# Kernel optimization log

Hardware: AMD Instinct MI355X
Metric: run time of the kernel (lower is better)

## Reference

```python
import jax, jax.numpy as jnp
import numpy as np

PI = float(np.pi)
BN_EPS = 1e-3
LN_EPS = 1e-5


def ssslu(x, shape, bias):
    # x * (sin(softsign(x) * shape*pi/2) + (bias + 1))
    s = x / (1.0 + jnp.abs(x))
    return x * (jnp.sin(s * (shape * PI / 2.0)) + (bias + 1.0))


def bn(x, g, b, m, v):
    inv = (g / jnp.sqrt(v + BN_EPS))[None, :, None, None]
    return (x - m[None, :, None, None]) * inv + b[None, :, None, None]


def conv2d(x, w, bias=None, pad=0):
    y = jax.lax.conv_general_dilated(x, w, (1, 1), [(pad, pad), (pad, pad)],
                                     dimension_numbers=('NCHW', 'OIHW', 'NCHW'))
    if bias is not None:
        y = y + bias[None, :, None, None]
    return y


def ln_silu(v):
    # LayerNorm (unit weight, zero bias) over last axis, then SiLU
    mu = jnp.mean(v, axis=-1, keepdims=True)
    var = jnp.mean(jnp.square(v - mu), axis=-1, keepdims=True)
    h = (v - mu) / jnp.sqrt(var + LN_EPS)
    return h * jax.nn.sigmoid(h)


def _forward(x, w_qkv, g_qkv, b_qkv, m_qkv, v_qkv,
             w_co, g_co, b_co, m_co, v_co,
             w_b1, bias_b1, g_b1, b_b1, m_b1, v_b1,
             w_b2, bias_b2, g_b2, b_b2, m_b2, v_b2):
    B, C, H, W = x.shape
    Q = (w_qkv.shape[0] - C) // 2
    # qkv Conv block: conv1x1 -> SSSLU(-3, 0.3) -> BN
    t = bn(ssslu(conv2d(x, w_qkv, pad=0), -3.0, 0.3), g_qkv, b_qkv, m_qkv, v_qkv)
    xq, xk, xv = jnp.split(t, [Q, 2 * Q], axis=1)
    # max-pooled Q/K rows and columns -> [B*Q, W] / [B*Q, H]
    qw = jnp.max(xq, axis=2).reshape(B * Q, W)
    kw = jnp.max(xk, axis=2).reshape(B * Q, W)
    qh = jnp.max(xq, axis=3).reshape(B * Q, H)
    kh = jnp.max(xk, axis=3).reshape(B * Q, H)
    # xaw[i,b] = max_a qw[i,a]*kw[i,b]; xah[i,a] = max_b qh[i,a]*kh[i,b]
    xaw = jnp.max(qw[:, :, None] * kw[:, None, :], axis=1)  # [BQ, W]
    xah = jnp.max(qh[:, :, None] * kh[:, None, :], axis=2)  # [BQ, H]
    xaw = ln_silu(xaw)
    xah = ln_silu(xah)
    xa = (xah[:, :, None] * xaw[:, None, :]).reshape(B, Q, H, W)
    # co: SSSLUConv(Q+C -> Q): conv3x3 -> BN -> SSSLU(1.0, 0)
    xa = jnp.concatenate([xa, xv], axis=1)
    xa = ssslu(bn(conv2d(xa, w_co, pad=1), g_co, b_co, m_co, v_co), 1.0, 0.0)
    # back[0]: Conv(Q -> C, k3, bias): conv -> SSSLU(-3, 0.3) -> BN
    xa = bn(ssslu(conv2d(xa, w_b1, bias_b1, pad=1), -3.0, 0.3), g_b1, b_b1, m_b1, v_b1)
    # back[1]: SSSLUConv(C -> C, k1, bias): conv -> BN -> SSSLU(0.8, 0)
    xa = ssslu(bn(conv2d(xa, w_b2, bias_b2, pad=0), g_b2, b_b2, m_b2, v_b2), 0.8, 0.0)
    # back[2]: Sigmoid; source returns the gate itself
    return jax.nn.sigmoid(xa)


def setup_inputs() -> dict:
    B, C, Q, H, W = 16, 256, 256, 64, 64
    key = jax.random.key(0)
    ks = jax.random.split(key, 32)

    def w_init(k, o, i, kh, kw):
        return jax.random.normal(k, (o, i, kh, kw), jnp.float32) * (1.0 / np.sqrt(i * kh * kw))

    def bn_params(k, c):
        k1, k2, k3, k4 = jax.random.split(k, 4)
        g = jax.random.uniform(k1, (c,), jnp.float32, 0.5, 1.5)
        b = jax.random.normal(k2, (c,), jnp.float32) * 0.1
        m = jax.random.normal(k3, (c,), jnp.float32) * 0.1
        v = jax.random.uniform(k4, (c,), jnp.float32, 0.5, 1.5)
        return g, b, m, v

    x = jax.random.normal(ks[0], (B, C, H, W), jnp.float32)
    w_qkv = w_init(ks[1], 2 * Q + C, C, 1, 1)
    g_qkv, b_qkv, m_qkv, v_qkv = bn_params(ks[2], 2 * Q + C)
    w_co = w_init(ks[3], Q, Q + C, 3, 3)
    g_co, b_co, m_co, v_co = bn_params(ks[4], Q)
    w_b1 = w_init(ks[5], C, Q, 3, 3)
    bias_b1 = jax.random.normal(ks[6], (C,), jnp.float32) * 0.05
    g_b1, b_b1, m_b1, v_b1 = bn_params(ks[7], C)
    w_b2 = w_init(ks[8], C, C, 1, 1)
    bias_b2 = jax.random.normal(ks[9], (C,), jnp.float32) * 0.05
    g_b2, b_b2, m_b2, v_b2 = bn_params(ks[10], C)
    return dict(x=x, w_qkv=w_qkv, g_qkv=g_qkv, b_qkv=b_qkv, m_qkv=m_qkv, v_qkv=v_qkv,
                w_co=w_co, g_co=g_co, b_co=b_co, m_co=m_co, v_co=v_co,
                w_b1=w_b1, bias_b1=bias_b1, g_b1=g_b1, b_b1=b_b1, m_b1=m_b1, v_b1=v_b1,
                w_b2=w_b2, bias_b2=bias_b2, g_b2=g_b2, b_b2=b_b2, m_b2=m_b2, v_b2=v_b2)


def reference(x, w_qkv, g_qkv, b_qkv, m_qkv, v_qkv,
              w_co, g_co, b_co, m_co, v_co,
              w_b1, bias_b1, g_b1, b_b1, m_b1, v_b1,
              w_b2, bias_b2, g_b2, b_b2, m_b2, v_b2):
    return _forward(x, w_qkv, g_qkv, b_qkv, m_qkv, v_qkv,
                    w_co, g_co, b_co, m_co, v_co,
                    w_b1, bias_b1, g_b1, b_b1, m_b1, v_b1,
                    w_b2, bias_b2, g_b2, b_b2, m_b2, v_b2)
```

## Files before the change

kernel.cpp:

```cpp
#include <hip/hip_runtime.h>
#include <hip/hip_bf16.h>
#include <math.h>

#define PI_F 3.14159265358979323846f

typedef unsigned short u16;
typedef unsigned int   u32;
typedef float    f32x4 __attribute__((ext_vector_type(4)));
typedef _Float16 f16x8 __attribute__((ext_vector_type(8)));
typedef u16      u16x8 __attribute__((ext_vector_type(8)));
typedef u16      u16x4 __attribute__((ext_vector_type(4)));

__device__ __forceinline__ u16 f2h(float f){ union{ _Float16 h; u16 u; } c; c.h = (_Float16)f; return c.u; }
__device__ __forceinline__ float h2f(u16 u){ union{ u16 u; _Float16 h; } c; c.u = u; return (float)c.h; }

__device__ __forceinline__ void gl16(const void* g, void* l){
  __builtin_amdgcn_global_load_lds((const __attribute__((address_space(1))) u32*)g,
                                   (__attribute__((address_space(3))) u32*)l, 16, 0, 0);
}

__device__ __forceinline__ int SWZ(int r){ return (r>>1)&3; }

__device__ __forceinline__ float wred_max(float v){
#pragma unroll
  for (int m = 32; m; m >>= 1) v = fmaxf(v, __shfl_xor(v, m));
  return v;
}
__device__ __forceinline__ float wred_min(float v){
#pragma unroll
  for (int m = 32; m; m >>= 1) v = fminf(v, __shfl_xor(v, m));
  return v;
}
__device__ __forceinline__ float wred_sum(float v){
#pragma unroll
  for (int m = 32; m; m >>= 1) v += __shfl_xor(v, m);
  return v;
}

__device__ __forceinline__ float ssslu_f(float x, float shp, float bp1){
  float s = x / (1.0f + fabsf(x));
  return x * (__sinf(s * shp) + bp1);
}

__device__ __forceinline__ float epi_val(float v, float4 p, float shp, float bp1, int ORDER, bool SIG){
  v += p.w;
  if (ORDER == 0){ v = ssslu_f(v, shp, bp1); v = (v - p.z) * p.x + p.y; }
  else           { v = (v - p.z) * p.x + p.y; v = ssslu_f(v, shp, bp1); }
  if (SIG) v = 1.f / (1.f + __expf(-v));
  return v;
}

__device__ __forceinline__ f16x8 mul8h(u16x8 a, u16x8 b){
  union{ u16x8 u; f16x8 h; } A, B; A.u = a; B.u = b;
  return A.h * B.h;
}

__global__ __launch_bounds__(256)
void xpose_k(const float* __restrict__ X, u16* __restrict__ XH)
{
  __shared__ u16 L[16384];
  const int tid = threadIdx.x;
  const int b = blockIdx.x >> 6, h = blockIdx.x & 63;
  const float* xp = X + (size_t)b * 256 * 4096 + h * 64;
#pragma unroll
  for (int i = 0; i < 16; ++i){
    int ci = i * 16 + (tid >> 4);
    int w4 = (tid & 15) * 4;
    float4 v = *(const float4*)(xp + (size_t)ci * 4096 + w4);
    int sw = 4 * ((ci >> 3) & 15);
    u16x4 d;
    d[0] = f2h(v.x); d[1] = f2h(v.y); d[2] = f2h(v.z); d[3] = f2h(v.w);
    *(u16x4*)&L[ci * 64 + (w4 ^ sw)] = d;
  }
  __syncthreads();
  u16* out = XH + (((size_t)b * 4096 + (size_t)h * 64) << 8);
#pragma unroll
  for (int it = 0; it < 8; ++it){
    int w   = it * 8 + (tid >> 5);
    int m   = tid & 31;
    int ci0 = m * 8;
    int base = (w & ~3) ^ (4 * (m & 15));
    int wl   = w & 3;
    u16x8 o;
#pragma unroll
    for (int k = 0; k < 8; ++k)
      o[k] = L[(ci0 + k) * 64 + base + wl];
    *(u16x8*)&out[w * 256 + ci0] = o;
  }
}

template<int CI_T, bool CAT>
__global__ __launch_bounds__(256, 2)
void conv3_mfma(const u16* __restrict__ Apk, const u16* __restrict__ Bg,
                u16* __restrict__ DstH, const float4* __restrict__ pp,
                const u16* __restrict__ xahT_, const u16* __restrict__ xawT_,
                float shp, float bp1, int ORDER)
{
  constexpr int NCC = CI_T / 32;
  constexpr int NIT = NCC * 3;
  __shared__ __align__(16) u16 sAB[37248];

  const int tid  = threadIdx.x;
  const int lane = tid & 63;
  const int wv   = tid >> 6;
  const int wn   = wv;
  const int l15  = lane & 15, l4 = lane >> 4;

  const int bx  = blockIdx.x;
  const int bid = (bx & 7) * 32 + (bx >> 3);
  const int b   = bid >> 4;
  const int r0  = (bid & 15) * 4;
  const int m0  = blockIdx.y * 128;

  if (tid < 192){
    int rr = tid >> 5, rem = tid & 31;
    int wp = (rem & 16) ? 65 : 0;
    *(u32*)&sAB[24576 + rr * 2112 + wp * 32 + (rem & 15) * 2] = 0;
  }
  if (r0 == 0)
    for (int i = tid; i < 1056; i += 256) *(u32*)&sAB[24576 + i * 2] = 0;
  if (r0 == 60)
    for (int i = tid; i < 1056; i += 256) *(u32*)&sAB[24576 + 5 * 2112 + i * 2] = 0;

  const int rA = tid >> 2, s4 = tid & 3;
  const u32 offA0 = ((u32)rA * CI_T + ((s4 ^ SWZ(rA)) << 3)) * 2;
  const u32 offA1 = ((u32)(rA + 64) * CI_T + ((s4 ^ SWZ(rA + 64)) << 3)) * 2;
  const u32 offB  = (((u32)rA << 8) + ((s4 ^ SWZ(rA + 1)) << 3)) * 2;

  auto STAGE_A = [&](int it2){
    int d2 = it2 % 3, c2 = it2 / 3;
    u16* dst = &sAB[(it2 & 1) * 12288 + wv * 512];
    const char* pa = (const char*)(Apk + ((size_t)(d2 * 3 * 256) + m0) * CI_T + c2 * 32);
#pragma unroll
    for (int j2 = 0; j2 < 3; ++j2){
      gl16(pa + offA0, dst + j2 * 4096);
      gl16(pa + offA1, dst + j2 * 4096 + 2048);
      pa += (size_t)256 * CI_T * 2;
    }
  };
  auto STAGE_B = [&](int c2){
#pragma unroll
    for (int j = 0; j < 6; ++j){
      int hh = r0 - 1 + j;
      if ((unsigned)hh >= 64u) continue;
      if (CAT && c2 < 8){
        int w = rA, s = s4;
        int ci0 = c2 * 32 + ((s ^ SWZ(w + 1)) << 3);
        u16x8 vh = *(const u16x8*)&xahT_[((b * 64 + hh) << 8) + ci0];
        u16x8 vw = *(const u16x8*)&xawT_[((b * 64 + w ) << 8) + ci0];
        *(f16x8*)&sAB[24576 + j * 2112 + (w + 1) * 32 + s * 8] = mul8h(vh, vw);
      } else {
        int cio = CAT ? (c2 * 32 - 256) : (c2 * 32);
        const char* pb = (const char*)(Bg + (((size_t)b * 4096 + (size_t)hh * 64) << 8) + cio);
        gl16(pb + offB, &sAB[24576 + j * 2112 + 32 + wv * 512]);
      }
    }
  };

  f32x4 acc[8][4];
#pragma unroll
  for (int i = 0; i < 8; ++i)
#pragma unroll
    for (int j = 0; j < 4; ++j){ acc[i][j][0]=0.f; acc[i][j][1]=0.f; acc[i][j][2]=0.f; acc[i][j][3]=0.f; }

  const char* lds = (const char*)sAB;
  const u32 aoff = (u32)l15 * 64 + (u32)((l4 ^ ((l15 >> 1) & 3)) << 4);
  const char* ab0 = lds + aoff;
  const char* ab1 = lds + aoff + 24576;
  const u32 bcom = 49152u + (u32)wn * 4224;
  const char* bb0 = lds + bcom + (u32)(l15 + 0) * 64 + (u32)((l4 ^ (((l15 + 0) >> 1) & 3)) << 4);
  const char* bb1 = lds + bcom + (u32)(l15 + 1) * 64 + (u32)((l4 ^ (((l15 + 1) >> 1) & 3)) << 4);
  const char* bb2 = lds + bcom + (u32)(l15 + 2) * 64 + (u32)((l4 ^ (((l15 + 2) >> 1) & 3)) << 4);

  STAGE_A(0);

  for (int c = 0; c < NCC; ++c){
#pragma unroll
    for (int d = 0; d < 3; ++d){
      const int it = 3 * c + d;
      if (it + 1 < NIT) STAGE_A(it + 1);
      if (d == 0){ STAGE_B(c); __syncthreads(); }

      const char* ab = ((c + d) & 1) ? ab1 : ab0;
#pragma unroll
      for (int dw = 0; dw < 3; ++dw){
        const char* bp = (dw == 0) ? bb0 : (dw == 1) ? bb1 : bb2;
        f16x8 afr[8], bfr[4];
#pragma unroll
        for (int fm = 0; fm < 8; ++fm)
          afr[fm] = *(const f16x8*)(ab + dw * 8192 + fm * 1024);
#pragma unroll
        for (int fn = 0; fn < 4; ++fn)
          bfr[fn] = *(const f16x8*)(bp + d * 4224 + fn * 1024);
        __builtin_amdgcn_s_setprio(1);
#pragma unroll
        for (int fm = 0; fm < 8; ++fm)
#pragma unroll
          for (int fn = 0; fn < 4; ++fn)
            acc[fm][fn] = __builtin_amdgcn_mfma_f32_16x16x32_f16(afr[fm], bfr[fn], acc[fm][fn], 0, 0, 0);
        __builtin_amdgcn_s_setprio(0);
      }
      __syncthreads();
    }
  }

  const int h = r0 + wn;
#pragma unroll
  for (int fm = 0; fm < 8; ++fm){
    const int cobase = m0 + fm * 16 + 4 * l4;
    float4 P0 = pp[cobase], P1 = pp[cobase+1], P2 = pp[cobase+2], P3 = pp[cobase+3];
#pragma unroll
    for (int fn = 0; fn < 4; ++fn){
      int w = fn * 16 + l15;
      float v0 = epi_val(acc[fm][fn][0], P0, shp, bp1, ORDER, false);
      float v1 = epi_val(acc[fm][fn][1], P1, shp, bp1, ORDER, false);
      float v2 = epi_val(acc[fm][fn][2], P2, shp, bp1, ORDER, false);
      float v3 = epi_val(acc[fm][fn][3], P3, shp, bp1, ORDER, false);
      uint2 st;
      st.x = (u32)f2h(v0) | ((u32)f2h(v1) << 16);
      st.y = (u32)f2h(v2) | ((u32)f2h(v3) << 16);
      *(uint2*)&DstH[(((size_t)b * 4096 + (size_t)h * 64 + w) << 8) + cobase] = st;
    }
  }
}

template<int EPI>
__global__ __launch_bounds__(512, 2)
void conv1_res(const u16* __restrict__ Apk0, const u16* __restrict__ Bg,
               u16* __restrict__ DstH, float* __restrict__ DstF,
               const float4* __restrict__ pp0,
               float* __restrict__ qhp, float* __restrict__ khp,
               float* __restrict__ qwp, float* __restrict__ kwp,
               float shp, float bp1, int ORDER)
{
  __shared__ __align__(16) u16 AL[65536];
  float* pool = (float*)AL;

  const int tid  = threadIdx.x;
  const int lane = tid & 63;
  const int wv   = tid >> 6;
  const int wm   = wv >> 2;
  const int wn   = wv & 3;
  const int l15  = lane & 15, l4 = lane >> 4;

  const int bx   = blockIdx.x;
  const int bid  = (bx & 7) * 32 + (bx >> 3);
  const int b    = bid >> 4;
  const int hblk = bid & 15;
  const int h0   = hblk * 4;
  const int m0   = (EPI == 0) ? (blockIdx.y * 256) : 0;

  const u16*    Apk = Apk0 + (size_t)m0 * 256;
  const float4* pp  = pp0 + m0;

  {
    const int g0 = tid;
    const int g1 = 512 + tid;
    const int mA0 = g0 >> 2, sA0 = g0 & 3;
    const int mA1 = g1 >> 2, sA1 = g1 & 3;
    const u32 offA0 = ((u32)mA0 * 256 + ((sA0 ^ SWZ(mA0)) << 3)) * 2;
    const u32 offA1 = ((u32)mA1 * 256 + ((sA1 ^ SWZ(mA1)) << 3)) * 2;
#pragma unroll
    for (int c = 0; c < 8; ++c){
      const char* pa = (const char*)(Apk + c * 32);
      gl16(pa + offA0, &AL[c * 8192 + (wv * 64) * 8]);
      gl16(pa + offA1, &AL[c * 8192 + (512 + wv * 64) * 8]);
    }
  }

  const u16* Bp = Bg + (((size_t)b * 4096 + (size_t)(h0 + wn) * 64) << 8) + (l15 << 8) + (l4 << 3);
#define LDB(c, fn) (*(const f16x8*)(Bp + ((fn) * 16 << 8) + (c) * 32))

  f32x4 acc[8][4];
#pragma unroll
  for (int i = 0; i < 8; ++i)
#pragma unroll
    for (int j = 0; j < 4; ++j){ acc[i][j][0]=0.f; acc[i][j][1]=0.f; acc[i][j][2]=0.f; acc[i][j][3]=0.f; }

  f16x8 bn0 = LDB(0, 0), bn1 = LDB(0, 1), bn2 = LDB(0, 2), bn3 = LDB(0, 3);

  __syncthreads();

  const char* abase = (const char*)AL + wm * 8192 + l15 * 64 + ((l4 ^ SWZ(l15)) << 4);

#pragma unroll
  for (int c = 0; c < 8; ++c){
    f16x8 b0 = bn0, b1 = bn1, b2 = bn2, b3 = bn3;
    if (c < 7){
      bn0 = LDB(c + 1, 0); bn1 = LDB(c + 1, 1); bn2 = LDB(c + 1, 2); bn3 = LDB(c + 1, 3);
    }
    f16x8 afr[8];
#pragma unroll
    for (int fm = 0; fm < 8; ++fm)
      afr[fm] = *(const f16x8*)(abase + c * 16384 + fm * 1024);
    __builtin_amdgcn_s_setprio(1);
#pragma unroll
    for (int fm = 0; fm < 8; ++fm){
      acc[fm][0] = __builtin_amdgcn_mfma_f32_16x16x32_f16(afr[fm], b0, acc[fm][0], 0, 0, 0);
      acc[fm][1] = __builtin_amdgcn_mfma_f32_16x16x32_f16(afr[fm], b1, acc[fm][1], 0, 0, 0);
      acc[fm][2] = __builtin_amdgcn_mfma_f32_16x16x32_f16(afr[fm], b2, acc[fm][2], 0, 0, 0);
      acc[fm][3] = __builtin_amdgcn_mfma_f32_16x16x32_f16(afr[fm], b3, acc[fm][3], 0, 0, 0);
    }
    __builtin_amdgcn_s_setprio(0);
  }
#undef LDB

  const int h = h0 + wn;

  if (EPI == 0){
    float* rowp = (blockIdx.y == 0) ? qhp : khp;
    float* colp = (blockIdx.y == 0) ? qwp : kwp;
    __syncthreads();
#pragma unroll
    for (int k = 0; k < 4; ++k){
      if (wn == k){
#pragma unroll
        for (int fm = 0; fm < 8; ++fm){
          const int cl = wm * 128 + fm * 16 + 4 * l4;
          float4 P0 = pp[cl], P1 = pp[cl+1], P2 = pp[cl+2], P3 = pp[cl+3];
          float ev[4][4];
#pragma unroll
          for (int fn = 0; fn < 4; ++fn){
            ev[fn][0] = epi_val(acc[fm][fn][0], P0, shp, bp1, 0, false);
            ev[fn][1] = epi_val(acc[fm][fn][1], P1, shp, bp1, 0, false);
            ev[fn][2] = epi_val(acc[fm][fn][2], P2, shp, bp1, 0, false);
            ev[fn][3] = epi_val(acc[fm][fn][3], P3, shp, bp1, 0, false);
          }
#pragma unroll
          for (int r = 0; r < 4; ++r){
            float mv = fmaxf(fmaxf(ev[0][r], ev[1][r]), fmaxf(ev[2][r], ev[3][r]));
            mv = fmaxf(mv, __shfl_xor(mv, 1));
            mv = fmaxf(mv, __shfl_xor(mv, 2));
            mv = fmaxf(mv, __shfl_xor(mv, 4));
            mv = fmaxf(mv, __shfl_xor(mv, 8));
            if (l15 == 0)
              rowp[(((b << 8) | (cl + r)) << 6) + h] = mv;
          }
#pragma unroll
          for (int fn = 0; fn < 4; ++fn)
#pragma unroll
            for (int r = 0; r < 4; ++r){
              int idx = ((cl + r) << 6) + fn * 16 + l15;
              pool[idx] = (k == 0) ? ev[fn][r] : fmaxf(pool[idx], ev[fn][r]);
            }
        }
      }
      __syncthreads();
    }
    float* cbase = colp + (((size_t)(b * 16 + hblk)) << 14);
#pragma unroll
    for (int j = 0; j < 8; ++j){
      int fi = j * 512 + tid;
      *(float4*)&cbase[fi * 4] = *(const float4*)&pool[fi * 4];
    }
  } else {
#pragma unroll
    for (int fm = 0; fm < 8; ++fm){
      const int cobase = wm * 128 + fm * 16 + 4 * l4;
      float4 P0 = pp[cobase], P1 = pp[cobase+1], P2 = pp[cobase+2], P3 = pp[cobase+3];
#pragma unroll
      for (int fn = 0; fn < 4; ++fn){
        int w = fn * 16 + l15;
        if (EPI == 1){
          float v0 = epi_val(acc[fm][fn][0], P0, shp, bp1, ORDER, false);
          float v1 = epi_val(acc[fm][fn][1], P1, shp, bp1, ORDER, false);
          float v2 = epi_val(acc[fm][fn][2], P2, shp, bp1, ORDER, false);
          float v3 = epi_val(acc[fm][fn][3], P3, shp, bp1, ORDER, false);
          uint2 st;
          st.x = (u32)f2h(v0) | ((u32)f2h(v1) << 16);
          st.y = (u32)f2h(v2) | ((u32)f2h(v3) << 16);
          *(uint2*)&DstH[(((size_t)b * 4096 + (size_t)h * 64 + w) << 8) + cobase] = st;
        } else {
          float v0 = epi_val(acc[fm][fn][0], P0, shp, bp1, ORDER, true);
          float v1 = epi_val(acc[fm][fn][1], P1, shp, bp1, ORDER, true);
          float v2 = epi_val(acc[fm][fn][2], P2, shp, bp1, ORDER, true);
          float v3 = epi_val(acc[fm][fn][3], P3, shp, bp1, ORDER, true);
          size_t base = ((size_t)(b * 256 + cobase)) * 4096 + (size_t)h * 64 + w;
          DstF[base]          = v0;
          DstF[base + 4096]   = v1;
          DstF[base + 2*4096] = v2;
          DstF[base + 3*4096] = v3;
        }
      }
    }
  }
}

__device__ __forceinline__ float ln_silu_wave(float v){
  float mu = wred_sum(v) * (1.f / 64.f);
  float d = v - mu;
  float var = wred_sum(d * d) * (1.f / 64.f);
  float hn = d * rsqrtf(var + 1e-5f);
  return hn / (1.f + __expf(-hn));
}

__global__ void attn_k(const float* __restrict__ qwp, const float* __restrict__ kwp,
                       const float* __restrict__ qh, const float* __restrict__ kh,
                       u16* __restrict__ xahT, u16* __restrict__ xawT)
{
  int row  = blockIdx.x * 4 + (threadIdx.x >> 6);
  int lane = threadIdx.x & 63;
  int idx  = (row << 6) + lane;
  int b = row >> 8, q = row & 255;
  size_t pb = ((size_t)b << 18) + (q << 6) + lane;
  float qwv = -3.0e38f, kwv = -3.0e38f;
#pragma unroll
  for (int hb = 0; hb < 16; ++hb){
    qwv = fmaxf(qwv, qwp[pb + ((size_t)hb << 14)]);
    kwv = fmaxf(kwv, kwp[pb + ((size_t)hb << 14)]);
  }
  float qhv = qh[idx], khv = kh[idx];
  float Pq = wred_max(qwv), mq = wred_min(qwv);
  float Pk = wred_max(khv), mk = wred_min(khv);
  float aw = fmaxf(kwv * Pq, kwv * mq);
  float ah = fmaxf(qhv * Pk, qhv * mk);
  aw = ln_silu_wave(aw);
  ah = ln_silu_wave(ah);
  xawT[((b * 64 + lane) << 8) + q] = f2h(aw);
  xahT[((b * 64 + lane) << 8) + q] = f2h(ah);
}

__global__ void pack_k(const float* __restrict__ wqkv, const float* __restrict__ wco,
                       const float* __restrict__ wb1, const float* __restrict__ wb2,
                       const float* gq, const float* bq, const float* mq, const float* vq,
                       const float* gc, const float* bc, const float* mc, const float* vc,
                       const float* g1, const float* b1, const float* m1, const float* v1, const float* bias1,
                       const float* g2, const float* b2, const float* m2, const float* v2, const float* bias2,
                       u16* __restrict__ WQ, u16* __restrict__ WCO, u16* __restrict__ WB1, u16* __restrict__ WB2,
                       float4* __restrict__ PP)
{
  const int E0 = 196608, E1 = 196608 + 1179648, E2 = 196608 + 1179648 + 589824, E3 = 2031616;
  int i = blockIdx.x * 256 + threadIdx.x;
  if (i >= E3 + 1536) return;
  if (i < E0){ WQ[i] = f2h(wqkv[i]); }
  else if (i < E1){
    int d = i - E0; int tap = d / 131072; int rm = d % 131072; int m = rm >> 9; int ci = rm & 511;
    WCO[d] = f2h(wco[(size_t)((m << 9) | ci) * 9 + tap]);
  } else if (i < E2){
    int d = i - E1; int tap = d / 65536; int rm = d & 65535; int m = rm >> 8; int ci = rm & 255;
    WB1[d] = f2h(wb1[(size_t)((m << 8) | ci) * 9 + tap]);
  } else if (i < E3){
    int d = i - E2; WB2[d] = f2h(wb2[d]);
  } else {
    int c = i - E3;
    float g, be, mm, vv, bi;
    if (c < 768){ g = gq[c]; be = bq[c]; mm = mq[c]; vv = vq[c]; bi = 0.f; }
    else if (c < 1024){ int j = c - 768;  g = gc[j]; be = bc[j]; mm = mc[j]; vv = vc[j]; bi = 0.f; }
    else if (c < 1280){ int j = c - 1024; g = g1[j]; be = b1[j]; mm = m1[j]; vv = v1[j]; bi = bias1[j]; }
    else              { int j = c - 1280; g = g2[j]; be = b2[j]; mm = m2[j]; vv = v2[j]; bi = bias2[j]; }
    PP[c] = make_float4(g / sqrtf(vv + 1e-3f), be, mm, bi);
  }
}

extern "C" void kernel_launch(void* const* d_in, const int* in_sizes, int n_in,
                              void* d_out, int out_size, void* d_ws, size_t ws_size,
                              hipStream_t stream)
{
  const float* x       = (const float*)d_in[0];
  const float* w_qkv   = (const float*)d_in[1];
  const float* g_qkv   = (const float*)d_in[2];
  const float* b_qkv   = (const float*)d_in[3];
  const float* m_qkv   = (const float*)d_in[4];
  const float* v_qkv   = (const float*)d_in[5];
  const float* w_co    = (const float*)d_in[6];
  const float* g_co    = (const float*)d_in[7];
  const float* b_co    = (const float*)d_in[8];
  const float* m_co    = (const float*)d_in[9];
  const float* v_co    = (const float*)d_in[10];
  const float* w_b1    = (const float*)d_in[11];
  const float* bias_b1 = (const float*)d_in[12];
  const float* g_b1    = (const float*)d_in[13];
  const float* b_b1    = (const float*)d_in[14];
  const float* m_b1    = (const float*)d_in[15];
  const float* v_b1    = (const float*)d_in[16];
  const float* w_b2    = (const float*)d_in[17];
  const float* bias_b2 = (const float*)d_in[18];
  const float* g_b2    = (const float*)d_in[19];
  const float* b_b2    = (const float*)d_in[20];
  const float* m_b2    = (const float*)d_in[21];
  const float* v_b2    = (const float*)d_in[22];
  float* out = (float*)d_out;

  char* W = (char*)d_ws;
  u16*    WQ   = (u16*)(W + 0);
  u16*    WCO  = (u16*)(W + 393216);
  u16*    WB1  = (u16*)(W + 2752512);
  u16*    WB2  = (u16*)(W + 3932160);
  float4* PP   = (float4*)(W + 4063232);
  float*  qwp_ = (float*)(W + 4087808);
  float*  kwp_ = (float*)(W + 20865024);
  u16*    TV   = (u16*)(W + 4087808);
  u16*    XAHT = (u16*)(W + 37642240);
  u16*    XAWT = (u16*)(W + 38166528);
  u16*    XH   = (u16*)(W + 38690816);
  u16*    Y1   = (u16*)(W + 38690816);
  u16*    Y2   = TV;
  float*  qh_  = (float*)(W + 72245248);
  float*  kh_  = (float*)(W + 73293824);

  const size_t NEED = 74342400;
  if (ws_size < NEED) return;

  const float SHP_N3 = -3.0f * PI_F * 0.5f;
  const float SHP_1  =  1.0f * PI_F * 0.5f;
  const float SHP_08 =  0.8f * PI_F * 0.5f;

  dim3 blk(256);

  pack_k<<<7942, blk, 0, stream>>>(w_qkv, w_co, w_b1, w_b2,
      g_qkv, b_qkv, m_qkv, v_qkv,
      g_co,  b_co,  m_co,  v_co,
      g_b1,  b_b1,  m_b1,  v_b1,  bias_b1,
      g_b2,  b_b2,  m_b2,  v_b2,  bias_b2,
      WQ, WCO, WB1, WB2, PP);

  xpose_k<<<1024, blk, 0, stream>>>(x, XH);

  conv1_res<0><<<dim3(256, 2), 512, 0, stream>>>(
      WQ, XH, nullptr, nullptr, PP, qh_, kh_, qwp_, kwp_, SHP_N3, 1.3f, 0);

  attn_k<<<1024, blk, 0, stream>>>(qwp_, kwp_, qh_, kh_, XAHT, XAWT);

  conv1_res<1><<<dim3(256, 1), 512, 0, stream>>>(
      WQ + (size_t)512 * 256, XH, TV, nullptr, PP + 512,
      nullptr, nullptr, nullptr, nullptr, SHP_N3, 1.3f, 0);

  conv3_mfma<512, true><<<dim3(256, 2), blk, 0, stream>>>(
      WCO, TV, Y1, PP + 768, XAHT, XAWT, SHP_1, 1.0f, 1);

  conv3_mfma<256, false><<<dim3(256, 2), blk, 0, stream>>>(
      WB1, Y1, Y2, PP + 1024, nullptr, nullptr, SHP_N3, 1.3f, 0);

  conv1_res<2><<<dim3(256, 1), 512, 0, stream>>>(
      WB2, Y2, nullptr, out, PP + 1280,
      nullptr, nullptr, nullptr, nullptr, SHP_08, 1.0f, 1);
}
```

Before: 439.6 us.

## Split Q/K max-pooling out of conv epilogue into separate pool kernels

Removes the fused row/column max-pooling from the first 1x1 conv epilogue. Q and K are now each written as fp16 tensors by the plain conv kernel, then reduced by new poolh_k and poolw_k kernels, and attn_k reads the final pooled vectors directly. This removes the serialized per-wave LDS pooling, the extra syncthreads and the large partial-column buffers, but adds conv launches, pool launches and an fp16 round trip of Q/K through memory. Pooling now runs on fp16-rounded values, which slightly changes numerics.

```diff
diff --git a/kernel.cpp b/kernel.cpp
--- a/kernel.cpp
+++ b/kernel.cpp
@@ -226,15 +226,12 @@
 
 template<int EPI>
 __global__ __launch_bounds__(512, 2)
-void conv1_res(const u16* __restrict__ Apk0, const u16* __restrict__ Bg,
+void conv1_res(const u16* __restrict__ Apk, const u16* __restrict__ Bg,
                u16* __restrict__ DstH, float* __restrict__ DstF,
-               const float4* __restrict__ pp0,
-               float* __restrict__ qhp, float* __restrict__ khp,
-               float* __restrict__ qwp, float* __restrict__ kwp,
+               const float4* __restrict__ pp,
                float shp, float bp1, int ORDER)
 {
   __shared__ __align__(16) u16 AL[65536];
-  float* pool = (float*)AL;
 
   const int tid  = threadIdx.x;
   const int lane = tid & 63;
@@ -246,12 +243,7 @@
   const int bx   = blockIdx.x;
   const int bid  = (bx & 7) * 32 + (bx >> 3);
   const int b    = bid >> 4;
-  const int hblk = bid & 15;
-  const int h0   = hblk * 4;
-  const int m0   = (EPI == 0) ? (blockIdx.y * 256) : 0;
-
-  const u16*    Apk = Apk0 + (size_t)m0 * 256;
-  const float4* pp  = pp0 + m0;
+  const int h0   = (bid & 15) * 4;
 
   {
     const int g0 = tid;
@@ -306,84 +298,89 @@
 #undef LDB
 
   const int h = h0 + wn;
-
-  if (EPI == 0){
-    float* rowp = (blockIdx.y == 0) ? qhp : khp;
-    float* colp = (blockIdx.y == 0) ? qwp : kwp;
-    __syncthreads();
-#pragma unroll
-    for (int k = 0; k < 4; ++k){
-      if (wn == k){
-#pragma unroll
-        for (int fm = 0; fm < 8; ++fm){
-          const int cl = wm * 128 + fm * 16 + 4 * l4;
-          float4 P0 = pp[cl], P1 = pp[cl+1], P2 = pp[cl+2], P3 = pp[cl+3];
-          float ev[4][4];
-#pragma unroll
-          for (int fn = 0; fn < 4; ++fn){
-            ev[fn][0] = epi_val(acc[fm][fn][0], P0, shp, bp1, 0, false);
-            ev[fn][1] = epi_val(acc[fm][fn][1], P1, shp, bp1, 0, false);
-            ev[fn][2] = epi_val(acc[fm][fn][2], P2, shp, bp1, 0, false);
-            ev[fn][3] = epi_val(acc[fm][fn][3], P3, shp, bp1, 0, false);
-          }
-#pragma unroll
-          for (int r = 0; r < 4; ++r){
-            float mv = fmaxf(fmaxf(ev[0][r], ev[1][r]), fmaxf(ev[2][r], ev[3][r]));
-            mv = fmaxf(mv, __shfl_xor(mv, 1));
-            mv = fmaxf(mv, __shfl_xor(mv, 2));
-            mv = fmaxf(mv, __shfl_xor(mv, 4));
-            mv = fmaxf(mv, __shfl_xor(mv, 8));
-            if (l15 == 0)
-              rowp[(((b << 8) | (cl + r)) << 6) + h] = mv;
-          }
-#pragma unroll
-          for (int fn = 0; fn < 4; ++fn)
-#pragma unroll
-            for (int r = 0; r < 4; ++r){
-              int idx = ((cl + r) << 6) + fn * 16 + l15;
-              pool[idx] = (k == 0) ? ev[fn][r] : fmaxf(pool[idx], ev[fn][r]);
-            }
-        }
+#pragma unroll
+  for (int fm = 0; fm < 8; ++fm){
+    const int cobase = wm * 128 + fm * 16 + 4 * l4;
+    float4 P0 = pp[cobase], P1 = pp[cobase+1], P2 = pp[cobase+2], P3 = pp[cobase+3];
+#pragma unroll
+    for (int fn = 0; fn < 4; ++fn){
+      int w = fn * 16 + l15;
+      if (EPI == 1){
+        float v0 = epi_val(acc[fm][fn][0], P0, shp, bp1, ORDER, false);
+        float v1 = epi_val(acc[fm][fn][1], P1, shp, bp1, ORDER, false);
+        float v2 = epi_val(acc[fm][fn][2], P2, shp, bp1, ORDER, false);
+        float v3 = epi_val(acc[fm][fn][3], P3, shp, bp1, ORDER, false);
+        uint2 st;
+        st.x = (u32)f2h(v0) | ((u32)f2h(v1) << 16);
+        st.y = (u32)f2h(v2) | ((u32)f2h(v3) << 16);
+        *(uint2*)&DstH[(((size_t)b * 4096 + (size_t)h * 64 + w) << 8) + cobase] = st;
+      } else {
+        float v0 = epi_val(acc[fm][fn][0], P0, shp, bp1, ORDER, true);
+        float v1 = epi_val(acc[fm][fn][1], P1, shp, bp1, ORDER, true);
+        float v2 = epi_val(acc[fm][fn][2], P2, shp, bp1, ORDER, true);
+        float v3 = epi_val(acc[fm][fn][3], P3, shp, bp1, ORDER, true);
+        size_t base = ((size_t)(b * 256 + cobase)) * 4096 + (size_t)h * 64 + w;
+        DstF[base]          = v0;
+        DstF[base + 4096]   = v1;
+        DstF[base + 2*4096] = v2;
+        DstF[base + 3*4096] = v3;
       }
-      __syncthreads();
-    }
-    float* cbase = colp + (((size_t)(b * 16 + hblk)) << 14);
-#pragma unroll
-    for (int j = 0; j < 8; ++j){
-      int fi = j * 512 + tid;
-      *(float4*)&cbase[fi * 4] = *(const float4*)&pool[fi * 4];
-    }
-  } else {
-#pragma unroll
-    for (int fm = 0; fm < 8; ++fm){
-      const int cobase = wm * 128 + fm * 16 + 4 * l4;
-      float4 P0 = pp[cobase], P1 = pp[cobase+1], P2 = pp[cobase+2], P3 = pp[cobase+3];
-#pragma unroll
-      for (int fn = 0; fn < 4; ++fn){
-        int w = fn * 16 + l15;
-        if (EPI == 1){
-          float v0 = epi_val(acc[fm][fn][0], P0, shp, bp1, ORDER, false);
-          float v1 = epi_val(acc[fm][fn][1], P1, shp, bp1, ORDER, false);
-          float v2 = epi_val(acc[fm][fn][2], P2, shp, bp1, ORDER, false);
-          float v3 = epi_val(acc[fm][fn][3], P3, shp, bp1, ORDER, false);
-          uint2 st;
-          st.x = (u32)f2h(v0) | ((u32)f2h(v1) << 16);
-          st.y = (u32)f2h(v2) | ((u32)f2h(v3) << 16);
-          *(uint2*)&DstH[(((size_t)b * 4096 + (size_t)h * 64 + w) << 8) + cobase] = st;
-        } else {
-          float v0 = epi_val(acc[fm][fn][0], P0, shp, bp1, ORDER, true);
-          float v1 = epi_val(acc[fm][fn][1], P1, shp, bp1, ORDER, true);
-          float v2 = epi_val(acc[fm][fn][2], P2, shp, bp1, ORDER, true);
-          float v3 = epi_val(acc[fm][fn][3], P3, shp, bp1, ORDER, true);
-          size_t base = ((size_t)(b * 256 + cobase)) * 4096 + (size_t)h * 64 + w;
-          DstF[base]          = v0;
-          DstF[base + 4096]   = v1;
-          DstF[base + 2*4096] = v2;
-          DstF[base + 3*4096] = v3;
-        }
-      }
-    }
-  }
+    }
+  }
+}
+
+__global__ __launch_bounds__(256)
+void poolh_k(const u16* __restrict__ T, float* __restrict__ rowp)
+{
+  __shared__ float L[8][256];
+  const int tid = threadIdx.x;
+  const int b = blockIdx.x >> 6, h = blockIdx.x & 63;
+  const int wg = tid >> 5;
+  const int c8 = (tid & 31) * 8;
+  const u16* base = T + (((size_t)b * 4096 + (size_t)h * 64) << 8) + c8;
+  float m[8];
+#pragma unroll
+  for (int e = 0; e < 8; ++e) m[e] = -3.0e38f;
+#pragma unroll
+  for (int j = 0; j < 8; ++j){
+    u16x8 v = *(const u16x8*)(base + ((wg * 8 + j) << 8));
+#pragma unroll
+    for (int e = 0; e < 8; ++e) m[e] = fmaxf(m[e], h2f(v[e]));
+  }
+#pragma unroll
+  for (int e = 0; e < 8; ++e) L[wg][c8 + e] = m[e];
+  __syncthreads();
+  const int c = tid;
+  float r = L[0][c];
+#pragma unroll
+  for (int g = 1; g < 8; ++g) r = fmaxf(r, L[g][c]);
+  rowp[(((b << 8) | c) << 6) + h] = r;
+}
+
+__global__ __launch_bounds__(256)
+void poolw_k(const u16* __restrict__ T, float* __restrict__ colp)
+{
+  __shared__ float L[4][256];
+  const int tid = threadIdx.x;
+  const int b = blockIdx.x >> 6, w = blockIdx.x & 63;
+  const int hs = tid >> 6;
+  const int c4 = (tid & 63) * 4;
+  const u16* base = T + (((size_t)b * 4096 + w) << 8) + c4;
+  float m0 = -3.0e38f, m1 = -3.0e38f, m2 = -3.0e38f, m3 = -3.0e38f;
+#pragma unroll
+  for (int hi = 0; hi < 16; ++hi){
+    int h = hi * 4 + hs;
+    u16x4 v = *(const u16x4*)(base + ((size_t)h << 14));
+    m0 = fmaxf(m0, h2f(v[0]));
+    m1 = fmaxf(m1, h2f(v[1]));
+    m2 = fmaxf(m2, h2f(v[2]));
+    m3 = fmaxf(m3, h2f(v[3]));
+  }
+  L[hs][c4 + 0] = m0; L[hs][c4 + 1] = m1; L[hs][c4 + 2] = m2; L[hs][c4 + 3] = m3;
+  __syncthreads();
+  const int c = tid;
+  float r = fmaxf(fmaxf(L[0][c], L[1][c]), fmaxf(L[2][c], L[3][c]));
+  colp[(((b << 8) | c) << 6) + w] = r;
 }
 
 __device__ __forceinline__ float ln_silu_wave(float v){
@@ -394,28 +391,21 @@
   return hn / (1.f + __expf(-hn));
 }
 
-__global__ void attn_k(const float* __restrict__ qwp, const float* __restrict__ kwp,
+__global__ void attn_k(const float* __restrict__ qw, const float* __restrict__ kw,
                        const float* __restrict__ qh, const float* __restrict__ kh,
                        u16* __restrict__ xahT, u16* __restrict__ xawT)
 {
   int row  = blockIdx.x * 4 + (threadIdx.x >> 6);
   int lane = threadIdx.x & 63;
   int idx  = (row << 6) + lane;
-  int b = row >> 8, q = row & 255;
-  size_t pb = ((size_t)b << 18) + (q << 6) + lane;
-  float qwv = -3.0e38f, kwv = -3.0e38f;
-#pragma unroll
-  for (int hb = 0; hb < 16; ++hb){
-    qwv = fmaxf(qwv, qwp[pb + ((size_t)hb << 14)]);
-    kwv = fmaxf(kwv, kwp[pb + ((size_t)hb << 14)]);
-  }
-  float qhv = qh[idx], khv = kh[idx];
+  float qwv = qw[idx], kwv = kw[idx], qhv = qh[idx], khv = kh[idx];
   float Pq = wred_max(qwv), mq = wred_min(qwv);
   float Pk = wred_max(khv), mk = wred_min(khv);
   float aw = fmaxf(kwv * Pq, kwv * mq);
   float ah = fmaxf(qhv * Pk, qhv * mk);
   aw = ln_silu_wave(aw);
   ah = ln_silu_wave(ah);
+  int b = row >> 8, q = row & 255;
   xawT[((b * 64 + lane) << 8) + q] = f2h(aw);
   xahT[((b * 64 + lane) << 8) + q] = f2h(ah);
 }
@@ -487,9 +477,8 @@
   u16*    WB1  = (u16*)(W + 2752512);
   u16*    WB2  = (u16*)(W + 3932160);
   float4* PP   = (float4*)(W + 4063232);
-  float*  qwp_ = (float*)(W + 4087808);
-  float*  kwp_ = (float*)(W + 20865024);
-  u16*    TV   = (u16*)(W + 4087808);
+  u16*    TQK  = (u16*)(W + 4087808);
+  u16*    TV   = TQK;
   u16*    XAHT = (u16*)(W + 37642240);
   u16*    XAWT = (u16*)(W + 38166528);
   u16*    XH   = (u16*)(W + 38690816);
@@ -497,8 +486,10 @@
   u16*    Y2   = TV;
   float*  qh_  = (float*)(W + 72245248);
   float*  kh_  = (float*)(W + 73293824);
-
-  const size_t NEED = 74342400;
+  float*  qw_  = (float*)(W + 74342400);
+  float*  kw_  = (float*)(W + 75390976);
+
+  const size_t NEED = 76439552;
   if (ws_size < NEED) return;
 
   const float SHP_N3 = -3.0f * PI_F * 0.5f;
@@ -516,14 +507,20 @@
 
   xpose_k<<<1024, blk, 0, stream>>>(x, XH);
 
-  conv1_res<0><<<dim3(256, 2), 512, 0, stream>>>(
-      WQ, XH, nullptr, nullptr, PP, qh_, kh_, qwp_, kwp_, SHP_N3, 1.3f, 0);
-
-  attn_k<<<1024, blk, 0, stream>>>(qwp_, kwp_, qh_, kh_, XAHT, XAWT);
-
-  conv1_res<1><<<dim3(256, 1), 512, 0, stream>>>(
-      WQ + (size_t)512 * 256, XH, TV, nullptr, PP + 512,
-      nullptr, nullptr, nullptr, nullptr, SHP_N3, 1.3f, 0);
+  conv1_res<1><<<256, 512, 0, stream>>>(
+      WQ, XH, TQK, nullptr, PP, SHP_N3, 1.3f, 0);
+  poolh_k<<<1024, blk, 0, stream>>>(TQK, qh_);
+  poolw_k<<<1024, blk, 0, stream>>>(TQK, qw_);
+
+  conv1_res<1><<<256, 512, 0, stream>>>(
+      WQ + (size_t)256 * 256, XH, TQK, nullptr, PP + 256, SHP_N3, 1.3f, 0);
+  poolh_k<<<1024, blk, 0, stream>>>(TQK, kh_);
+  poolw_k<<<1024, blk, 0, stream>>>(TQK, kw_);
+
+  attn_k<<<1024, blk, 0, stream>>>(qw_, kw_, qh_, kh_, XAHT, XAWT);
+
+  conv1_res<1><<<256, 512, 0, stream>>>(
+      WQ + (size_t)512 * 256, XH, TV, nullptr, PP + 512, SHP_N3, 1.3f, 0);
 
   conv3_mfma<512, true><<<dim3(256, 2), blk, 0, stream>>>(
       WCO, TV, Y1, PP + 768, XAHT, XAWT, SHP_1, 1.0f, 1);
@@ -531,7 +528,6 @@
   conv3_mfma<256, false><<<dim3(256, 2), blk, 0, stream>>>(
       WB1, Y1, Y2, PP + 1024, nullptr, nullptr, SHP_N3, 1.3f, 0);
 
-  conv1_res<2><<<dim3(256, 1), 512, 0, stream>>>(
-      WB2, Y2, nullptr, out, PP + 1280,
-      nullptr, nullptr, nullptr, nullptr, SHP_08, 1.0f, 1);
-}
+  conv1_res<2><<<256, 512, 0, stream>>>(
+      WB2, Y2, nullptr, out, PP + 1280, SHP_08, 1.0f, 1);
+}
```

Measured after the change: 376.9 us. -14.3%, faster.
